# Kernel tuning notes

Measured on AMD Instinct MI355X. Metric: run time of the kernel, lower is better.

The kernel has to match this reference:

```python
import jax, jax.numpy as jnp
import numpy as np

T, B, V, F = 30, 32, 32, 128   # len_pred, batch, n_vehicles, feature_size
L, LF = 256, 64                # n_lanes, lane_feature_size
H = 8                          # n_heads
DH = F // H                    # head dim
HIST = 10                      # leading mask dim reduced by any()


def setup_inputs() -> dict:
    key = jax.random.key(0)
    ks = jax.random.split(key, 16)
    s = 0.05
    return {
        "vehicles":    jax.random.normal(ks[0], (T, B, V, F), jnp.float32),
        "initial_pos": jax.random.normal(ks[1], (T, B, V, F), jnp.float32),
        "lanes":       jax.random.normal(ks[2], (B, L, LF), jnp.float32),
        "mask_lanes":  jax.random.randint(ks[3], (HIST, B, L), 0, 2).astype(bool),
        # key_lanes / value_lanes: Linear(LF -> F)
        "Wk": jax.random.normal(ks[4], (F, LF), jnp.float32) * s,
        "bk": jax.random.normal(ks[5], (F,), jnp.float32) * s,
        "Wv": jax.random.normal(ks[6], (F, LF), jnp.float32) * s,
        "bv": jax.random.normal(ks[7], (F,), jnp.float32) * s,
        # query / relation_lanes: Conv2d(F, F, (1,1)) == pointwise Linear(F -> F)
        "Wq": jax.random.normal(ks[8], (F, F), jnp.float32) * s,
        "bq": jax.random.normal(ks[9], (F,), jnp.float32) * s,
        "Wr": jax.random.normal(ks[10], (F, F), jnp.float32) * s,
        "br": jax.random.normal(ks[11], (F,), jnp.float32) * s,
        # attention_combine: Linear(F -> F)
        "Wc": jax.random.normal(ks[12], (F, F), jnp.float32) * s,
        "bc": jax.random.normal(ks[13], (F,), jnp.float32) * s,
    }


def reference(vehicles, initial_pos, lanes, mask_lanes,
              Wk, bk, Wv, bv, Wq, bq, Wr, br, Wc, bc):
    v = vehicles + initial_pos                                   # [T,B,V,F]
    # lane projections -> [B,H,L,DH]
    k = (lanes @ Wk.T + bk).reshape(B, L, H, DH).transpose(0, 2, 1, 3)
    val = (lanes @ Wv.T + bv).reshape(B, L, H, DH).transpose(0, 2, 1, 3)
    # vehicle projections (1x1 conv == linear over feature dim) -> [T,B,H,V,DH]
    q = (v @ Wq.T + bq).reshape(T, B, V, H, DH).transpose(0, 1, 3, 2, 4)
    r = (v @ Wr.T + br).reshape(T, B, V, H, DH).transpose(0, 1, 3, 2, 4)
    # mask: any over leading dims -> [B,L]
    mask = jnp.any(mask_lanes, axis=0)
    scores = jnp.einsum('tbhvd,bhld->tbhvl', q, k) / jnp.sqrt(jnp.float32(DH))
    scores = jnp.where(mask[None, :, None, None, :], scores, jnp.float32(-1e9))
    p = jax.nn.softmax(scores, axis=-1)                          # [T,B,H,V,L]
    att = jnp.exp(jnp.einsum('tbhvl,bhld->tbhvd', p, jax.nn.log_sigmoid(val)))
    # faithful to original: raw reshape [T,B,H,V,DH] -> [T,B,V,F] (no permute back)
    out = (r * att).reshape(T, B, V, F)
    return out @ Wc.T + bc + v - 2.0 * initial_pos
```

## Files before the change

kernel.cpp:

```cpp
#include <hip/hip_runtime.h>
#include <hip/hip_bf16.h>
#include <math.h>

#define T_ 30
#define B_ 32
#define V_ 32
#define F_ 128
#define L_ 256
#define LF_ 64
#define H_ 8
#define DH_ 16
#define HIST_ 10

typedef __attribute__((ext_vector_type(4))) float floatx4;
typedef __attribute__((ext_vector_type(8))) short shortx8;
typedef __attribute__((ext_vector_type(4))) unsigned short ushortx4;

#define MFMA_BF16(a, b, c) __builtin_amdgcn_mfma_f32_16x16x32_bf16(a, b, c, 0, 0, 0)

__device__ inline unsigned short f2bf_rne(float x) {
    unsigned int u = __builtin_bit_cast(unsigned int, x);
    unsigned int r = (u + 0x7fffu + ((u >> 16) & 1u)) >> 16;
    return (unsigned short)r;
}
__device__ inline unsigned short f2bf_trunc(float x) {
    return (unsigned short)(__builtin_bit_cast(unsigned int, x) >> 16);
}
__device__ inline float bf2f(unsigned short u) {
    return __builtin_bit_cast(float, (unsigned int)u << 16);
}
__device__ inline ushortx4 cvt4(floatx4 a) {
    ushortx4 r;
    r.x = f2bf_rne(a.x); r.y = f2bf_rne(a.y);
    r.z = f2bf_rne(a.z); r.w = f2bf_rne(a.w);
    return r;
}

__global__ __launch_bounds__(256, 2) void k_lanes(
    const float* __restrict__ lanes, const int* __restrict__ mask,
    const float* __restrict__ Wk, const float* __restrict__ bk,
    const float* __restrict__ Wv, const float* __restrict__ bv,
    unsigned short* __restrict__ kproj, unsigned short* __restrict__ lsvT,
    float* __restrict__ maskb) {
    __shared__ unsigned short WkF[8192];
    __shared__ unsigned short WvF[8192];
    __shared__ float mloc[64];
    int tid = threadIdx.x;
    int m0 = blockIdx.x * 64;
    int b = m0 >> 8;
    if (tid < 64) {
        int row = m0 + tid;
        int any = 0;
#pragma unroll
        for (int hh = 0; hh < HIST_; ++hh) any |= mask[hh * (B_ * L_) + row];
        float fm = any ? 1.0f : 0.0f;
        maskb[row] = fm;
        mloc[tid] = fm;
    }
    for (int g = tid; g < 1024; g += 256) {
        int frag = g >> 6, l = g & 63, cc = l & 15, qq = l >> 4;
        int nt = frag >> 1, ks = frag & 1;
        int n = nt * 16 + cc, k0 = ks * 32 + qq * 8;
        floatx4 a0 = *(const floatx4*)(Wk + n * LF_ + k0);
        floatx4 a1 = *(const floatx4*)(Wk + n * LF_ + k0 + 4);
        *(ushortx4*)(WkF + g * 8) = cvt4(a0);
        *(ushortx4*)(WkF + g * 8 + 4) = cvt4(a1);
        floatx4 b0 = *(const floatx4*)(Wv + n * LF_ + k0);
        floatx4 b1 = *(const floatx4*)(Wv + n * LF_ + k0 + 4);
        *(ushortx4*)(WvF + g * 8) = cvt4(b0);
        *(ushortx4*)(WvF + g * 8 + 4) = cvt4(b1);
    }
    __syncthreads();
    int lane = tid & 63, w = tid >> 6;
    int c = lane & 15, quad = lane >> 4;
    int mw = m0 + w * 16;
    shortx8 aF[2];
#pragma unroll
    for (int ks = 0; ks < 2; ++ks) {
        const float* xp = lanes + (size_t)(mw + c) * LF_ + ks * 32 + quad * 8;
        floatx4 x0 = *(const floatx4*)(xp);
        floatx4 x1 = *(const floatx4*)(xp + 4);
        ushortx4 lo = cvt4(x0), hi = cvt4(x1);
        shortx8 af;
        af[0]=(short)lo.x; af[1]=(short)lo.y; af[2]=(short)lo.z; af[3]=(short)lo.w;
        af[4]=(short)hi.x; af[5]=(short)hi.y; af[6]=(short)hi.z; af[7]=(short)hi.w;
        aF[ks] = af;
    }
    floatx4 mk = *(const floatx4*)(mloc + w * 16 + quad * 4);
    int lbase = (mw & 255) + quad * 4;
#pragma unroll
    for (int nt = 0; nt < 8; ++nt) {
        floatx4 acck = {0.f, 0.f, 0.f, 0.f}, accv = {0.f, 0.f, 0.f, 0.f};
#pragma unroll
        for (int ks = 0; ks < 2; ++ks) {
            shortx8 bkf = *(const shortx8*)(WkF + ((nt * 2 + ks) * 64 + lane) * 8);
            shortx8 bvf = *(const shortx8*)(WvF + ((nt * 2 + ks) * 64 + lane) * 8);
            acck = MFMA_BF16(aF[ks], bkf, acck);
            accv = MFMA_BF16(aF[ks], bvf, accv);
        }
        int n = nt * 16 + c;
        float bkn = bk[n], bvn = bv[n];
        ushortx4 vout;
#pragma unroll
        for (int reg = 0; reg < 4; ++reg) {
            size_t row = mw + quad * 4 + reg;
            kproj[row * F_ + n] = f2bf_rne(acck[reg] + bkn);
            float xv = accv[reg] + bvn;
            float ls = fminf(xv, 0.f) - log1pf(__expf(-fabsf(xv)));
            vout[reg] = (mk[reg] > 0.5f) ? f2bf_rne(ls) : (unsigned short)0;
        }
        *(ushortx4*)(lsvT + ((size_t)b * F_ + n) * L_ + lbase) = vout;
    }
}

__global__ __launch_bounds__(256, 2) void k_qr(
    const float* __restrict__ veh, const float* __restrict__ ip,
    const float* __restrict__ Wq, const float* __restrict__ bq,
    const float* __restrict__ Wr, const float* __restrict__ br,
    unsigned short* __restrict__ qb, unsigned short* __restrict__ rb) {
    __shared__ unsigned short WqF[16384];
    __shared__ unsigned short WrF[16384];
    int tid = threadIdx.x;
    for (int g = tid; g < 2048; g += 256) {
        int frag = g >> 6, l = g & 63, cc = l & 15, qq = l >> 4;
        int nt = frag >> 2, ks = frag & 3;
        int n = nt * 16 + cc, k0 = ks * 32 + qq * 8;
        floatx4 a0 = *(const floatx4*)(Wq + n * F_ + k0);
        floatx4 a1 = *(const floatx4*)(Wq + n * F_ + k0 + 4);
        *(ushortx4*)(WqF + g * 8) = cvt4(a0);
        *(ushortx4*)(WqF + g * 8 + 4) = cvt4(a1);
        floatx4 b0 = *(const floatx4*)(Wr + n * F_ + k0);
        floatx4 b1 = *(const floatx4*)(Wr + n * F_ + k0 + 4);
        *(ushortx4*)(WrF + g * 8) = cvt4(b0);
        *(ushortx4*)(WrF + g * 8 + 4) = cvt4(b1);
    }
    __syncthreads();
    int lane = tid & 63, w = tid >> 6;
    int c = lane & 15, quad = lane >> 4;
    int m0 = blockIdx.x * 64 + w * 16;
    shortx8 aF[4];
#pragma unroll
    for (int ks = 0; ks < 4; ++ks) {
        size_t off = (size_t)(m0 + c) * F_ + ks * 32 + quad * 8;
        floatx4 v0 = *(const floatx4*)(veh + off);
        floatx4 v1 = *(const floatx4*)(veh + off + 4);
        floatx4 i0 = *(const floatx4*)(ip + off);
        floatx4 i1 = *(const floatx4*)(ip + off + 4);
        ushortx4 lo = cvt4(v0 + i0), hi = cvt4(v1 + i1);
        shortx8 af;
        af[0]=(short)lo.x; af[1]=(short)lo.y; af[2]=(short)lo.z; af[3]=(short)lo.w;
        af[4]=(short)hi.x; af[5]=(short)hi.y; af[6]=(short)hi.z; af[7]=(short)hi.w;
        aF[ks] = af;
    }
    const float QSCALE = 0.25f * 1.4426950408889634f;
#pragma unroll
    for (int nt = 0; nt < 8; ++nt) {
        floatx4 accq = {0.f, 0.f, 0.f, 0.f}, accr = {0.f, 0.f, 0.f, 0.f};
#pragma unroll
        for (int ks = 0; ks < 4; ++ks) {
            shortx8 bqf = *(const shortx8*)(WqF + ((nt * 4 + ks) * 64 + lane) * 8);
            shortx8 brf = *(const shortx8*)(WrF + ((nt * 4 + ks) * 64 + lane) * 8);
            accq = MFMA_BF16(aF[ks], bqf, accq);
            accr = MFMA_BF16(aF[ks], brf, accr);
        }
        int n = nt * 16 + c;
        float bqn = bq[n], brn = br[n];
#pragma unroll
        for (int reg = 0; reg < 4; ++reg) {
            size_t row = m0 + quad * 4 + reg;
            qb[row * F_ + n] = f2bf_rne((accq[reg] + bqn) * QSCALE);
            rb[row * F_ + n] = f2bf_rne(accr[reg] + brn);
        }
    }
}

__global__ __launch_bounds__(256, 2) void k_attn(
    const unsigned short* __restrict__ kproj, const unsigned short* __restrict__ lsvT,
    const float* __restrict__ maskb, const unsigned short* __restrict__ qbuf,
    const unsigned short* __restrict__ rbuf, unsigned short* __restrict__ ratt) {
    __shared__ unsigned short kS[256 * 24];
    __shared__ unsigned short vT[16 * 264];
    __shared__ unsigned short pE[4 * 16 * 264];

    int tid = threadIdx.x;
    int bh = blockIdx.x & 255;
    int tc = blockIdx.x >> 8;
    int h = bh & 7;
    int b = bh >> 3;

    const unsigned short* kbase = kproj + ((size_t)b * L_) * F_ + h * DH_;
#pragma unroll
    for (int it = 0; it < 2; ++it) {
        int id = it * 256 + tid;
        int l = id >> 1, half = id & 1;
        shortx8 kv = *(const shortx8*)(kbase + (size_t)l * F_ + half * 8);
        *(shortx8*)(kS + l * 24 + half * 8) = kv;
    }
    {
        int d = tid >> 4, c16 = tid & 15;
        const unsigned short* vrow = lsvT + ((size_t)b * F_ + h * DH_ + d) * L_ + c16 * 16;
        shortx8 v0 = *(const shortx8*)(vrow);
        shortx8 v1 = *(const shortx8*)(vrow + 8);
        *(shortx8*)(vT + d * 264 + c16 * 16) = v0;
        *(shortx8*)(vT + d * 264 + c16 * 16 + 8) = v1;
    }
    __syncthreads();

    int lane = tid & 63, w = tid >> 6;
    int c = lane & 15, quad = lane >> 4;

    shortx8 kF[16];
#pragma unroll
    for (int lt = 0; lt < 16; ++lt) {
        shortx8 z = {0, 0, 0, 0, 0, 0, 0, 0};
        kF[lt] = (quad < 2) ? *(const shortx8*)(kS + (lt * 16 + c) * 24 + quad * 8) : z;
    }
    shortx8 vF[8];
#pragma unroll
    for (int kk = 0; kk < 8; ++kk)
        vF[kk] = *(const shortx8*)(vT + c * 264 + kk * 32 + quad * 8);
    shortx8 mF[8];
#pragma unroll
    for (int kk = 0; kk < 8; ++kk) {
        const float* mp = maskb + b * L_ + kk * 32 + quad * 8;
        floatx4 ma = *(const floatx4*)(mp);
        floatx4 mb2 = *(const floatx4*)(mp + 4);
        shortx8 mf;
        mf[0]=(short)f2bf_trunc(ma.x); mf[1]=(short)f2bf_trunc(ma.y);
        mf[2]=(short)f2bf_trunc(ma.z); mf[3]=(short)f2bf_trunc(ma.w);
        mf[4]=(short)f2bf_trunc(mb2.x); mf[5]=(short)f2bf_trunc(mb2.y);
        mf[6]=(short)f2bf_trunc(mb2.z); mf[7]=(short)f2bf_trunc(mb2.w);
        mF[kk] = mf;
    }

    unsigned short* pEw = pE + w * (16 * 264);
    floatx4 z4 = {0.f, 0.f, 0.f, 0.f};

    for (int mtl = w; mtl < 15; mtl += 4) {
        int mt = tc * 15 + mtl;
        int q0 = mt << 4;
        int t = q0 >> 5, v0 = q0 & 31;
        size_t qrow0 = ((size_t)(t * B_ + b) * V_ + v0 + c) * F_ + h * DH_;

        shortx8 qF = {0, 0, 0, 0, 0, 0, 0, 0};
        if (quad < 2) qF = *(const shortx8*)(qbuf + qrow0 + quad * 8);

#pragma unroll
        for (int lt = 0; lt < 16; ++lt) {
            floatx4 s = MFMA_BF16(kF[lt], qF, z4);
            ushortx4 ep;
#pragma unroll
            for (int reg = 0; reg < 4; ++reg)
                ep[reg] = f2bf_trunc(__builtin_amdgcn_exp2f(s[reg]));
            *(ushortx4*)(pEw + c * 264 + lt * 16 + quad * 4) = ep;
        }

        floatx4 cU = z4, cN = z4;
#pragma unroll
        for (int kk = 0; kk < 8; ++kk) {
            shortx8 bP = *(const shortx8*)(pEw + c * 264 + kk * 32 + quad * 8);
            cU = MFMA_BF16(vF[kk], bP, cU);
            cN = MFMA_BF16(mF[kk], bP, cN);
        }
        float inv2 = __builtin_amdgcn_rcpf(cN[0]) * 1.4426950408889634f;
        ushortx4 rv = *(const ushortx4*)(rbuf + qrow0 + quad * 4);
        ushortx4 ob;
#pragma unroll
        for (int reg = 0; reg < 4; ++reg) {
            float att = __builtin_amdgcn_exp2f(cU[reg] * inv2);
            ob[reg] = f2bf_rne(bf2f(rv[reg]) * att);
        }
        *(ushortx4*)(ratt + (((size_t)t * B_ + b) * H_ + h) * (V_ * DH_)
                    + (v0 + c) * DH_ + quad * 4) = ob;
    }
}

__global__ __launch_bounds__(256, 2) void k_out(
    const unsigned short* __restrict__ ratt, const float* __restrict__ Wc,
    const float* __restrict__ bc, const float* __restrict__ veh,
    const float* __restrict__ ip, float* __restrict__ out) {
    __shared__ unsigned short WcF[16384];
    int tid = threadIdx.x;
    for (int g = tid; g < 2048; g += 256) {
        int frag = g >> 6, l = g & 63, cc = l & 15, qq = l >> 4;
        int nt = frag >> 2, ks = frag & 3;
        int n = nt * 16 + cc, k0 = ks * 32 + qq * 8;
        floatx4 a0 = *(const floatx4*)(Wc + n * F_ + k0);
        floatx4 a1 = *(const floatx4*)(Wc + n * F_ + k0 + 4);
        *(ushortx4*)(WcF + g * 8) = cvt4(a0);
        *(ushortx4*)(WcF + g * 8 + 4) = cvt4(a1);
    }
    __syncthreads();
    int lane = tid & 63, w = tid >> 6;
    int c = lane & 15, quad = lane >> 4;
    int m0 = blockIdx.x * 64 + w * 16;
    shortx8 aF[4];
#pragma unroll
    for (int ks = 0; ks < 4; ++ks)
        aF[ks] = *(const shortx8*)(ratt + (size_t)(m0 + c) * F_ + ks * 32 + quad * 8);
#pragma unroll
    for (int np = 0; np < 4; ++np) {
        int nt0 = np * 2, nt1 = np * 2 + 1;
        floatx4 acc0 = {0.f, 0.f, 0.f, 0.f}, acc1 = {0.f, 0.f, 0.f, 0.f};
#pragma unroll
        for (int ks = 0; ks < 4; ++ks) {
            shortx8 b0 = *(const shortx8*)(WcF + ((nt0 * 4 + ks) * 64 + lane) * 8);
            shortx8 b1 = *(const shortx8*)(WcF + ((nt1 * 4 + ks) * 64 + lane) * 8);
            acc0 = MFMA_BF16(aF[ks], b0, acc0);
            acc1 = MFMA_BF16(aF[ks], b1, acc1);
        }
        int n0 = nt0 * 16 + c, n1 = nt1 * 16 + c;
        float bc0 = bc[n0], bc1 = bc[n1];
#pragma unroll
        for (int reg = 0; reg < 4; ++reg) {
            size_t row = m0 + quad * 4 + reg;
            size_t o0 = row * F_ + n0, o1 = row * F_ + n1;
            out[o0] = acc0[reg] + bc0 + veh[o0] - ip[o0];
            out[o1] = acc1[reg] + bc1 + veh[o1] - ip[o1];
        }
    }
}

extern "C" void kernel_launch(void* const* d_in, const int* in_sizes, int n_in,
                              void* d_out, int out_size, void* d_ws, size_t ws_size,
                              hipStream_t stream) {
    const float* vehicles    = (const float*)d_in[0];
    const float* initial_pos = (const float*)d_in[1];
    const float* lanes       = (const float*)d_in[2];
    const int*   mask        = (const int*)d_in[3];
    const float* Wk = (const float*)d_in[4];
    const float* bk = (const float*)d_in[5];
    const float* Wv = (const float*)d_in[6];
    const float* bv = (const float*)d_in[7];
    const float* Wq = (const float*)d_in[8];
    const float* bq = (const float*)d_in[9];
    const float* Wr = (const float*)d_in[10];
    const float* br = (const float*)d_in[11];
    const float* Wc = (const float*)d_in[12];
    const float* bc = (const float*)d_in[13];
    float* out = (float*)d_out;

    char* p = (char*)d_ws;
    float* maskb = (float*)p;                   p += ((B_ * L_ * 4 + 255) / 256) * 256;
    unsigned short* kproj = (unsigned short*)p; p += ((size_t)B_ * L_ * F_ * 2 + 255) / 256 * 256;
    unsigned short* lsvT  = (unsigned short*)p; p += ((size_t)B_ * F_ * L_ * 2 + 255) / 256 * 256;
    unsigned short* qb    = (unsigned short*)p; p += ((size_t)T_ * B_ * V_ * F_ * 2 + 255) / 256 * 256;
    unsigned short* rb    = (unsigned short*)p; p += ((size_t)T_ * B_ * V_ * F_ * 2 + 255) / 256 * 256;
    unsigned short* rattb = (unsigned short*)p; p += ((size_t)T_ * B_ * V_ * F_ * 2 + 255) / 256 * 256;

    k_lanes<<<(B_ * L_) / 64, 256, 0, stream>>>(lanes, mask, Wk, bk, Wv, bv, kproj, lsvT, maskb);
    k_qr<<<(T_ * B_ * V_) / 64, 256, 0, stream>>>(vehicles, initial_pos, Wq, bq, Wr, br, qb, rb);
    k_attn<<<4 * B_ * H_, 256, 0, stream>>>(kproj, lsvT, maskb, qb, rb, rattb);
    k_out<<<(T_ * B_ * V_) / 64, 256, 0, stream>>>(rattb, Wc, bc, vehicles, initial_pos, out);
}
```

Before: 168.3 us.

## Merge lane and vehicle projection kernels, cache bf16 residual, relayout P buffer

Folds the lane-projection and Q/R-projection kernels into one launch that splits work by block index, removing a kernel boundary. The projection kernel now also writes vehicles minus initial_pos as a bf16 residual, so the output kernel reads one half-width tensor instead of two fp32 tensors. The attention kernel's per-wave probability buffer is reorganised into MFMA-fragment order so the B operand becomes a contiguous per-lane load instead of a padded strided one. The residual is rounded to bf16, which costs accuracy, and the extra residual write adds traffic to the projection stage.

New measurement: 148.1 us. 12.0% less time.

```diff
diff --git a/kernel.cpp b/kernel.cpp
--- a/kernel.cpp
+++ b/kernel.cpp
@@ -36,140 +36,143 @@
     return r;
 }
 
-__global__ __launch_bounds__(256, 2) void k_lanes(
+__global__ __launch_bounds__(256, 2) void k_proj(
     const float* __restrict__ lanes, const int* __restrict__ mask,
+    const float* __restrict__ veh, const float* __restrict__ ip,
     const float* __restrict__ Wk, const float* __restrict__ bk,
     const float* __restrict__ Wv, const float* __restrict__ bv,
+    const float* __restrict__ Wq, const float* __restrict__ bq,
+    const float* __restrict__ Wr, const float* __restrict__ br,
     unsigned short* __restrict__ kproj, unsigned short* __restrict__ lsvT,
-    float* __restrict__ maskb) {
-    __shared__ unsigned short WkF[8192];
-    __shared__ unsigned short WvF[8192];
+    float* __restrict__ maskb, unsigned short* __restrict__ qb,
+    unsigned short* __restrict__ rb, unsigned short* __restrict__ resid) {
+    __shared__ unsigned short smem[32768];
     __shared__ float mloc[64];
     int tid = threadIdx.x;
-    int m0 = blockIdx.x * 64;
-    int b = m0 >> 8;
-    if (tid < 64) {
-        int row = m0 + tid;
-        int any = 0;
-#pragma unroll
-        for (int hh = 0; hh < HIST_; ++hh) any |= mask[hh * (B_ * L_) + row];
-        float fm = any ? 1.0f : 0.0f;
-        maskb[row] = fm;
-        mloc[tid] = fm;
-    }
-    for (int g = tid; g < 1024; g += 256) {
-        int frag = g >> 6, l = g & 63, cc = l & 15, qq = l >> 4;
-        int nt = frag >> 1, ks = frag & 1;
-        int n = nt * 16 + cc, k0 = ks * 32 + qq * 8;
-        floatx4 a0 = *(const floatx4*)(Wk + n * LF_ + k0);
-        floatx4 a1 = *(const floatx4*)(Wk + n * LF_ + k0 + 4);
-        *(ushortx4*)(WkF + g * 8) = cvt4(a0);
-        *(ushortx4*)(WkF + g * 8 + 4) = cvt4(a1);
-        floatx4 b0 = *(const floatx4*)(Wv + n * LF_ + k0);
-        floatx4 b1 = *(const floatx4*)(Wv + n * LF_ + k0 + 4);
-        *(ushortx4*)(WvF + g * 8) = cvt4(b0);
-        *(ushortx4*)(WvF + g * 8 + 4) = cvt4(b1);
-    }
-    __syncthreads();
-    int lane = tid & 63, w = tid >> 6;
-    int c = lane & 15, quad = lane >> 4;
-    int mw = m0 + w * 16;
-    shortx8 aF[2];
-#pragma unroll
-    for (int ks = 0; ks < 2; ++ks) {
-        const float* xp = lanes + (size_t)(mw + c) * LF_ + ks * 32 + quad * 8;
-        floatx4 x0 = *(const floatx4*)(xp);
-        floatx4 x1 = *(const floatx4*)(xp + 4);
-        ushortx4 lo = cvt4(x0), hi = cvt4(x1);
-        shortx8 af;
-        af[0]=(short)lo.x; af[1]=(short)lo.y; af[2]=(short)lo.z; af[3]=(short)lo.w;
-        af[4]=(short)hi.x; af[5]=(short)hi.y; af[6]=(short)hi.z; af[7]=(short)hi.w;
-        aF[ks] = af;
-    }
-    floatx4 mk = *(const floatx4*)(mloc + w * 16 + quad * 4);
-    int lbase = (mw & 255) + quad * 4;
-#pragma unroll
-    for (int nt = 0; nt < 8; ++nt) {
-        floatx4 acck = {0.f, 0.f, 0.f, 0.f}, accv = {0.f, 0.f, 0.f, 0.f};
+
+    if (blockIdx.x < 128) {
+        unsigned short* WkF = smem;
+        unsigned short* WvF = smem + 8192;
+        int m0 = blockIdx.x * 64;
+        int b = m0 >> 8;
+        if (tid < 64) {
+            int row = m0 + tid;
+            int any = 0;
+#pragma unroll
+            for (int hh = 0; hh < HIST_; ++hh) any |= mask[hh * (B_ * L_) + row];
+            float fm = any ? 1.0f : 0.0f;
+            maskb[row] = fm;
+            mloc[tid] = fm;
+        }
+        for (int g = tid; g < 1024; g += 256) {
+            int frag = g >> 6, l = g & 63, cc = l & 15, qq = l >> 4;
+            int nt = frag >> 1, ks = frag & 1;
+            int n = nt * 16 + cc, k0 = ks * 32 + qq * 8;
+            floatx4 a0 = *(const floatx4*)(Wk + n * LF_ + k0);
+            floatx4 a1 = *(const floatx4*)(Wk + n * LF_ + k0 + 4);
+            *(ushortx4*)(WkF + g * 8) = cvt4(a0);
+            *(ushortx4*)(WkF + g * 8 + 4) = cvt4(a1);
+            floatx4 b0 = *(const floatx4*)(Wv + n * LF_ + k0);
+            floatx4 b1 = *(const floatx4*)(Wv + n * LF_ + k0 + 4);
+            *(ushortx4*)(WvF + g * 8) = cvt4(b0);
+            *(ushortx4*)(WvF + g * 8 + 4) = cvt4(b1);
+        }
+        __syncthreads();
+        int lane = tid & 63, w = tid >> 6;
+        int c = lane & 15, quad = lane >> 4;
+        int mw = m0 + w * 16;
+        shortx8 aF[2];
 #pragma unroll
         for (int ks = 0; ks < 2; ++ks) {
-            shortx8 bkf = *(const shortx8*)(WkF + ((nt * 2 + ks) * 64 + lane) * 8);
-            shortx8 bvf = *(const shortx8*)(WvF + ((nt * 2 + ks) * 64 + lane) * 8);
-            acck = MFMA_BF16(aF[ks], bkf, acck);
-            accv = MFMA_BF16(aF[ks], bvf, accv);
-        }
-        int n = nt * 16 + c;
-        float bkn = bk[n], bvn = bv[n];
-        ushortx4 vout;
-#pragma unroll
-        for (int reg = 0; reg < 4; ++reg) {
-            size_t row = mw + quad * 4 + reg;
-            kproj[row * F_ + n] = f2bf_rne(acck[reg] + bkn);
-            float xv = accv[reg] + bvn;
-            float ls = fminf(xv, 0.f) - log1pf(__expf(-fabsf(xv)));
-            vout[reg] = (mk[reg] > 0.5f) ? f2bf_rne(ls) : (unsigned short)0;
-        }
-        *(ushortx4*)(lsvT + ((size_t)b * F_ + n) * L_ + lbase) = vout;
-    }
-}
-
-__global__ __launch_bounds__(256, 2) void k_qr(
-    const float* __restrict__ veh, const float* __restrict__ ip,
-    const float* __restrict__ Wq, const float* __restrict__ bq,
-    const float* __restrict__ Wr, const float* __restrict__ br,
-    unsigned short* __restrict__ qb, unsigned short* __restrict__ rb) {
-    __shared__ unsigned short WqF[16384];
-    __shared__ unsigned short WrF[16384];
-    int tid = threadIdx.x;
-    for (int g = tid; g < 2048; g += 256) {
-        int frag = g >> 6, l = g & 63, cc = l & 15, qq = l >> 4;
-        int nt = frag >> 2, ks = frag & 3;
-        int n = nt * 16 + cc, k0 = ks * 32 + qq * 8;
-        floatx4 a0 = *(const floatx4*)(Wq + n * F_ + k0);
-        floatx4 a1 = *(const floatx4*)(Wq + n * F_ + k0 + 4);
-        *(ushortx4*)(WqF + g * 8) = cvt4(a0);
-        *(ushortx4*)(WqF + g * 8 + 4) = cvt4(a1);
-        floatx4 b0 = *(const floatx4*)(Wr + n * F_ + k0);
-        floatx4 b1 = *(const floatx4*)(Wr + n * F_ + k0 + 4);
-        *(ushortx4*)(WrF + g * 8) = cvt4(b0);
-        *(ushortx4*)(WrF + g * 8 + 4) = cvt4(b1);
-    }
-    __syncthreads();
-    int lane = tid & 63, w = tid >> 6;
-    int c = lane & 15, quad = lane >> 4;
-    int m0 = blockIdx.x * 64 + w * 16;
-    shortx8 aF[4];
-#pragma unroll
-    for (int ks = 0; ks < 4; ++ks) {
-        size_t off = (size_t)(m0 + c) * F_ + ks * 32 + quad * 8;
-        floatx4 v0 = *(const floatx4*)(veh + off);
-        floatx4 v1 = *(const floatx4*)(veh + off + 4);
-        floatx4 i0 = *(const floatx4*)(ip + off);
-        floatx4 i1 = *(const floatx4*)(ip + off + 4);
-        ushortx4 lo = cvt4(v0 + i0), hi = cvt4(v1 + i1);
-        shortx8 af;
-        af[0]=(short)lo.x; af[1]=(short)lo.y; af[2]=(short)lo.z; af[3]=(short)lo.w;
-        af[4]=(short)hi.x; af[5]=(short)hi.y; af[6]=(short)hi.z; af[7]=(short)hi.w;
-        aF[ks] = af;
-    }
-    const float QSCALE = 0.25f * 1.4426950408889634f;
-#pragma unroll
-    for (int nt = 0; nt < 8; ++nt) {
-        floatx4 accq = {0.f, 0.f, 0.f, 0.f}, accr = {0.f, 0.f, 0.f, 0.f};
+            const float* xp = lanes + (size_t)(mw + c) * LF_ + ks * 32 + quad * 8;
+            floatx4 x0 = *(const floatx4*)(xp);
+            floatx4 x1 = *(const floatx4*)(xp + 4);
+            ushortx4 lo = cvt4(x0), hi = cvt4(x1);
+            shortx8 af;
+            af[0]=(short)lo.x; af[1]=(short)lo.y; af[2]=(short)lo.z; af[3]=(short)lo.w;
+            af[4]=(short)hi.x; af[5]=(short)hi.y; af[6]=(short)hi.z; af[7]=(short)hi.w;
+            aF[ks] = af;
+        }
+        floatx4 mk = *(const floatx4*)(mloc + w * 16 + quad * 4);
+        int lbase = (mw & 255) + quad * 4;
+#pragma unroll
+        for (int nt = 0; nt < 8; ++nt) {
+            floatx4 acck = {0.f, 0.f, 0.f, 0.f}, accv = {0.f, 0.f, 0.f, 0.f};
+#pragma unroll
+            for (int ks = 0; ks < 2; ++ks) {
+                shortx8 bkf = *(const shortx8*)(WkF + ((nt * 2 + ks) * 64 + lane) * 8);
+                shortx8 bvf = *(const shortx8*)(WvF + ((nt * 2 + ks) * 64 + lane) * 8);
+                acck = MFMA_BF16(aF[ks], bkf, acck);
+                accv = MFMA_BF16(aF[ks], bvf, accv);
+            }
+            int n = nt * 16 + c;
+            float bkn = bk[n], bvn = bv[n];
+            ushortx4 vout;
+#pragma unroll
+            for (int reg = 0; reg < 4; ++reg) {
+                size_t row = mw + quad * 4 + reg;
+                kproj[row * F_ + n] = f2bf_rne(acck[reg] + bkn);
+                float xv = accv[reg] + bvn;
+                float ls = fminf(xv, 0.f) - log1pf(__expf(-fabsf(xv)));
+                vout[reg] = (mk[reg] > 0.5f) ? f2bf_rne(ls) : (unsigned short)0;
+            }
+            *(ushortx4*)(lsvT + ((size_t)b * F_ + n) * L_ + lbase) = vout;
+        }
+    } else {
+        unsigned short* WqF = smem;
+        unsigned short* WrF = smem + 16384;
+        for (int g = tid; g < 2048; g += 256) {
+            int frag = g >> 6, l = g & 63, cc = l & 15, qq = l >> 4;
+            int nt = frag >> 2, ks = frag & 3;
+            int n = nt * 16 + cc, k0 = ks * 32 + qq * 8;
+            floatx4 a0 = *(const floatx4*)(Wq + n * F_ + k0);
+            floatx4 a1 = *(const floatx4*)(Wq + n * F_ + k0 + 4);
+            *(ushortx4*)(WqF + g * 8) = cvt4(a0);
+            *(ushortx4*)(WqF + g * 8 + 4) = cvt4(a1);
+            floatx4 b0 = *(const floatx4*)(Wr + n * F_ + k0);
+            floatx4 b1 = *(const floatx4*)(Wr + n * F_ + k0 + 4);
+            *(ushortx4*)(WrF + g * 8) = cvt4(b0);
+            *(ushortx4*)(WrF + g * 8 + 4) = cvt4(b1);
+        }
+        __syncthreads();
+        int lane = tid & 63, w = tid >> 6;
+        int c = lane & 15, quad = lane >> 4;
+        int m0 = (blockIdx.x - 128) * 64 + w * 16;
+        shortx8 aF[4];
 #pragma unroll
         for (int ks = 0; ks < 4; ++ks) {
-            shortx8 bqf = *(const shortx8*)(WqF + ((nt * 4 + ks) * 64 + lane) * 8);
-            shortx8 brf = *(const shortx8*)(WrF + ((nt * 4 + ks) * 64 + lane) * 8);
-            accq = MFMA_BF16(aF[ks], bqf, accq);
-            accr = MFMA_BF16(aF[ks], brf, accr);
-        }
-        int n = nt * 16 + c;
-        float bqn = bq[n], brn = br[n];
-#pragma unroll
-        for (int reg = 0; reg < 4; ++reg) {
-            size_t row = m0 + quad * 4 + reg;
-            qb[row * F_ + n] = f2bf_rne((accq[reg] + bqn) * QSCALE);
-            rb[row * F_ + n] = f2bf_rne(accr[reg] + brn);
+            size_t off = (size_t)(m0 + c) * F_ + ks * 32 + quad * 8;
+            floatx4 v0 = *(const floatx4*)(veh + off);
+            floatx4 v1 = *(const floatx4*)(veh + off + 4);
+            floatx4 i0 = *(const floatx4*)(ip + off);
+            floatx4 i1 = *(const floatx4*)(ip + off + 4);
+            ushortx4 lo = cvt4(v0 + i0), hi = cvt4(v1 + i1);
+            shortx8 af;
+            af[0]=(short)lo.x; af[1]=(short)lo.y; af[2]=(short)lo.z; af[3]=(short)lo.w;
+            af[4]=(short)hi.x; af[5]=(short)hi.y; af[6]=(short)hi.z; af[7]=(short)hi.w;
+            aF[ks] = af;
+            *(ushortx4*)(resid + off) = cvt4(v0 - i0);
+            *(ushortx4*)(resid + off + 4) = cvt4(v1 - i1);
+        }
+        const float QSCALE = 0.25f * 1.4426950408889634f;
+#pragma unroll
+        for (int nt = 0; nt < 8; ++nt) {
+            floatx4 accq = {0.f, 0.f, 0.f, 0.f}, accr = {0.f, 0.f, 0.f, 0.f};
+#pragma unroll
+            for (int ks = 0; ks < 4; ++ks) {
+                shortx8 bqf = *(const shortx8*)(WqF + ((nt * 4 + ks) * 64 + lane) * 8);
+                shortx8 brf = *(const shortx8*)(WrF + ((nt * 4 + ks) * 64 + lane) * 8);
+                accq = MFMA_BF16(aF[ks], bqf, accq);
+                accr = MFMA_BF16(aF[ks], brf, accr);
+            }
+            int n = nt * 16 + c;
+            float bqn = bq[n], brn = br[n];
+#pragma unroll
+            for (int reg = 0; reg < 4; ++reg) {
+                size_t row = m0 + quad * 4 + reg;
+                qb[row * F_ + n] = f2bf_rne((accq[reg] + bqn) * QSCALE);
+                rb[row * F_ + n] = f2bf_rne(accr[reg] + brn);
+            }
         }
     }
 }
@@ -180,7 +183,7 @@
     const unsigned short* __restrict__ rbuf, unsigned short* __restrict__ ratt) {
     __shared__ unsigned short kS[256 * 24];
     __shared__ unsigned short vT[16 * 264];
-    __shared__ unsigned short pE[4 * 16 * 264];
+    __shared__ unsigned short pE[4 * 4096];
 
     int tid = threadIdx.x;
     int bh = blockIdx.x & 255;
@@ -233,7 +236,9 @@
         mF[kk] = mf;
     }
 
-    unsigned short* pEw = pE + w * (16 * 264);
+    unsigned short* pEw = pE + w * 4096;
+    int wr_c = c * 8 + (quad & 1) * 4;
+    int wr_q = (quad >> 1) * 128;
     floatx4 z4 = {0.f, 0.f, 0.f, 0.f};
 
     for (int mtl = w; mtl < 15; mtl += 4) {
@@ -252,13 +257,13 @@
 #pragma unroll
             for (int reg = 0; reg < 4; ++reg)
                 ep[reg] = f2bf_trunc(__builtin_amdgcn_exp2f(s[reg]));
-            *(ushortx4*)(pEw + c * 264 + lt * 16 + quad * 4) = ep;
+            *(ushortx4*)(pEw + (lt >> 1) * 512 + (lt & 1) * 256 + wr_q + wr_c) = ep;
         }
 
         floatx4 cU = z4, cN = z4;
 #pragma unroll
         for (int kk = 0; kk < 8; ++kk) {
-            shortx8 bP = *(const shortx8*)(pEw + c * 264 + kk * 32 + quad * 8);
+            shortx8 bP = *(const shortx8*)(pEw + (kk * 64 + lane) * 8);
             cU = MFMA_BF16(vF[kk], bP, cU);
             cN = MFMA_BF16(mF[kk], bP, cN);
         }
@@ -277,8 +282,8 @@
 
 __global__ __launch_bounds__(256, 2) void k_out(
     const unsigned short* __restrict__ ratt, const float* __restrict__ Wc,
-    const float* __restrict__ bc, const float* __restrict__ veh,
-    const float* __restrict__ ip, float* __restrict__ out) {
+    const float* __restrict__ bc, const unsigned short* __restrict__ resid,
+    float* __restrict__ out) {
     __shared__ unsigned short WcF[16384];
     int tid = threadIdx.x;
     for (int g = tid; g < 2048; g += 256) {
@@ -315,8 +320,8 @@
         for (int reg = 0; reg < 4; ++reg) {
             size_t row = m0 + quad * 4 + reg;
             size_t o0 = row * F_ + n0, o1 = row * F_ + n1;
-            out[o0] = acc0[reg] + bc0 + veh[o0] - ip[o0];
-            out[o1] = acc1[reg] + bc1 + veh[o1] - ip[o1];
+            out[o0] = acc0[reg] + bc0 + bf2f(resid[o0]);
+            out[o1] = acc1[reg] + bc1 + bf2f(resid[o1]);
         }
     }
 }
@@ -347,9 +352,11 @@
     unsigned short* qb    = (unsigned short*)p; p += ((size_t)T_ * B_ * V_ * F_ * 2 + 255) / 256 * 256;
     unsigned short* rb    = (unsigned short*)p; p += ((size_t)T_ * B_ * V_ * F_ * 2 + 255) / 256 * 256;
     unsigned short* rattb = (unsigned short*)p; p += ((size_t)T_ * B_ * V_ * F_ * 2 + 255) / 256 * 256;
-
-    k_lanes<<<(B_ * L_) / 64, 256, 0, stream>>>(lanes, mask, Wk, bk, Wv, bv, kproj, lsvT, maskb);
-    k_qr<<<(T_ * B_ * V_) / 64, 256, 0, stream>>>(vehicles, initial_pos, Wq, bq, Wr, br, qb, rb);
+    unsigned short* resid = (unsigned short*)p; p += ((size_t)T_ * B_ * V_ * F_ * 2 + 255) / 256 * 256;
+
+    k_proj<<<128 + (T_ * B_ * V_) / 64, 256, 0, stream>>>(
+        lanes, mask, vehicles, initial_pos, Wk, bk, Wv, bv, Wq, bq, Wr, br,
+        kproj, lsvT, maskb, qb, rb, resid);
     k_attn<<<4 * B_ * H_, 256, 0, stream>>>(kproj, lsvT, maskb, qb, rb, rattb);
-    k_out<<<(T_ * B_ * V_) / 64, 256, 0, stream>>>(rattb, Wc, bc, vehicles, initial_pos, out);
-}
+    k_out<<<(T_ * B_ * V_) / 64, 256, 0, stream>>>(rattb, Wc, bc, resid, out);
+}
```
